# Kernel optimization log

Measured on AMD Instinct MI355X. Metric: run time of the kernel, lower is better.

## Reference

```python
import jax, jax.numpy as jnp
import numpy as np

N, T = 8192, 8192
RB, CB = 32, 32
HID = 100


def setup_inputs() -> dict:
    key = jax.random.key(0)
    ks = jax.random.split(key, 10)
    X = jax.random.normal(ks[0], (N, T), dtype=jnp.float32)
    # sorted segment ids emulate the multinomial block partition (row/col cumsum boundaries)
    row_ids = jnp.sort(jax.random.randint(ks[1], (N,), 0, RB)).astype(jnp.int32)
    col_ids = jnp.sort(jax.random.randint(ks[2], (T,), 0, CB)).astype(jnp.int32)
    d_io = RB * CB
    s1 = 1.0 / np.sqrt(d_io)
    s2 = 1.0 / np.sqrt(HID)
    W1 = jax.random.uniform(ks[3], (d_io, HID), jnp.float32, -s1, s1)
    b1 = jnp.zeros((HID,), jnp.float32)
    W2 = jax.random.uniform(ks[4], (HID, HID), jnp.float32, -s2, s2)
    b2 = jnp.zeros((HID,), jnp.float32)
    W3 = jax.random.uniform(ks[5], (HID, d_io), jnp.float32, -s2, s2)
    b3 = jnp.zeros((d_io,), jnp.float32)
    return {"X": X, "row_ids": row_ids, "col_ids": col_ids,
            "W1": W1, "b1": b1, "W2": W2, "b2": b2, "W3": W3, "b3": b3}


def _block_mean(X, row_ids, col_ids):
    # single-pass segmented reduce replacing the nested Python loop over blocks
    row_sum = jax.ops.segment_sum(X, row_ids, num_segments=RB)            # [RB, T]
    blk_sum = jax.ops.segment_sum(row_sum.T, col_ids, num_segments=CB).T  # [RB, CB]
    rcnt = jnp.bincount(row_ids, length=RB).astype(jnp.float32)
    ccnt = jnp.bincount(col_ids, length=CB).astype(jnp.float32)
    cnt = jnp.maximum(rcnt[:, None] * ccnt[None, :], 1.0)
    return blk_sum / cnt


def _mar_mlp(x_small, W1, b1, W2, b2, W3, b3):
    # 3-layer relu MLP propensity generator (MAR_missingness), sigmoid output
    h = x_small.reshape(-1)
    h = jax.nn.relu(h @ W1 + b1)
    h = jax.nn.relu(h @ W2 + b2)
    return jax.nn.sigmoid(h @ W3 + b3).reshape(RB, CB)


def reference(X, row_ids, col_ids, W1, b1, W2, b2, W3, b3):
    X_small = _block_mean(X, row_ids, col_ids)
    propensity = _mar_mlp(X_small, W1, b1, W2, b2, W3, b3)
    row_cumsum = jnp.concatenate([jnp.zeros((1,), jnp.int32),
                                  jnp.cumsum(jnp.bincount(row_ids, length=RB)).astype(jnp.int32)])
    col_cumsum = jnp.concatenate([jnp.zeros((1,), jnp.int32),
                                  jnp.cumsum(jnp.bincount(col_ids, length=CB)).astype(jnp.int32)])
    return propensity, row_cumsum, col_cumsum
```

## Files before the change

### kernel.cpp

```cpp
#include <hip/hip_runtime.h>
#include <math.h>

#define N 8192
#define T 8192
#define RB 32
#define CB 32
#define HID 100
#define DIO (RB*CB)

#define RPB 8
#define BS_BLOCKS (N / RPB)
#define K1BLOCKS 32
#define KCHUNK (DIO/K1BLOCKS)

__global__ void k_bounds(const int* __restrict__ row_ids, const int* __restrict__ col_ids,
                         int* __restrict__ rc, int* __restrict__ cc, float* __restrict__ blk) {
    int tid = blockIdx.x * blockDim.x + threadIdx.x;
    int stride = gridDim.x * blockDim.x;
    for (int i = tid; i < DIO; i += stride) blk[i] = 0.f;
    for (int i = tid; i < N; i += stride) {
        int a = row_ids[i];
        int b = (i + 1 < N) ? row_ids[i + 1] : RB;
        for (int k = a + 1; k <= b; ++k) rc[k] = i + 1;
        if (i == 0) { for (int k = 0; k <= a; ++k) rc[k] = 0; }
    }
    for (int i = tid; i < T; i += stride) {
        int a = col_ids[i];
        int b = (i + 1 < T) ? col_ids[i + 1] : CB;
        for (int k = a + 1; k <= b; ++k) cc[k] = i + 1;
        if (i == 0) { for (int k = 0; k <= a; ++k) cc[k] = 0; }
    }
}

__device__ __forceinline__ void flush_seg(float4* acc, const int4* __restrict__ col_ids4,
                                          int t, int rs, float* __restrict__ blk) {
    const int lane = t & 63;
    #pragma unroll
    for (int j = 0; j < 8; ++j) {
        int4 cs = col_ids4[t + 256 * j];
        int key = cs.x;
        float v;
        if (cs.w == key) {
            v = acc[j].x + acc[j].y + acc[j].z + acc[j].w;
        } else {
            v = acc[j].x;
            if (cs.y == key) v += acc[j].y; else atomicAdd(&blk[rs * CB + cs.y], acc[j].y);
            if (cs.z == key) v += acc[j].z; else atomicAdd(&blk[rs * CB + cs.z], acc[j].z);
            if (cs.w == key) v += acc[j].w; else atomicAdd(&blk[rs * CB + cs.w], acc[j].w);
        }
        #pragma unroll
        for (int d = 1; d < 64; d <<= 1) {
            float vv = __shfl_down(v, d, 64);
            int   kk = __shfl_down(key, d, 64);
            if (lane + d < 64 && kk == key) v += vv;
        }
        int kprev = __shfl_up(key, 1, 64);
        if (lane == 0 || kprev != key)
            atomicAdd(&blk[rs * CB + key], v);
        acc[j] = make_float4(0.f, 0.f, 0.f, 0.f);
    }
}

__global__ __launch_bounds__(256) void k_blocksum(const float* __restrict__ X,
        const int* __restrict__ row_ids, const int* __restrict__ col_ids,
        float* __restrict__ blk) {
    const int t = threadIdx.x;
    const int b = blockIdx.x;
    const int r0 = b * RPB;
    const float4* __restrict__ X4 = (const float4*)X;
    const int4*   __restrict__ C4 = (const int4*)col_ids;

    float4 acc[8];
    #pragma unroll
    for (int j = 0; j < 8; ++j) acc[j] = make_float4(0.f, 0.f, 0.f, 0.f);

    const int4* rid4 = (const int4*)(row_ids + r0);
    int4 ra = rid4[0], rb = rid4[1];

    if (ra.x == rb.w) {
        #pragma unroll
        for (int r = 0; r < RPB; ++r) {
            const float4* __restrict__ row = X4 + (size_t)(r0 + r) * (T / 4);
            #pragma unroll
            for (int j = 0; j < 8; ++j) {
                float4 x = row[t + 256 * j];
                acc[j].x += x.x; acc[j].y += x.y; acc[j].z += x.z; acc[j].w += x.w;
            }
        }
        flush_seg(acc, C4, t, ra.x, blk);
    } else {
        int rseg[RPB] = {ra.x, ra.y, ra.z, ra.w, rb.x, rb.y, rb.z, rb.w};
        int cur = rseg[0];
        for (int r = 0; r < RPB; ++r) {
            if (rseg[r] != cur) { flush_seg(acc, C4, t, cur, blk); cur = rseg[r]; }
            const float4* __restrict__ row = X4 + (size_t)(r0 + r) * (T / 4);
            #pragma unroll
            for (int j = 0; j < 8; ++j) {
                float4 x = row[t + 256 * j];
                acc[j].x += x.x; acc[j].y += x.y; acc[j].z += x.z; acc[j].w += x.w;
            }
        }
        flush_seg(acc, C4, t, cur, blk);
    }
}

__global__ __launch_bounds__(128) void k_mlp1(const float* __restrict__ blk,
        const int* __restrict__ rc, const int* __restrict__ cc,
        const float* __restrict__ W1, float* __restrict__ part1) {
    __shared__ float xs[KCHUNK];
    const int b = blockIdx.x, t = threadIdx.x;
    const int k0 = b * KCHUNK;
    if (t < KCHUNK) {
        int k = k0 + t;
        int r = k >> 5, c = k & 31;
        float cnt = fmaxf((float)(rc[r + 1] - rc[r]) * (float)(cc[c + 1] - cc[c]), 1.0f);
        xs[t] = blk[k] / cnt;
    }
    __syncthreads();
    if (t < HID) {
        float s = 0.f;
        #pragma unroll 8
        for (int kk = 0; kk < KCHUNK; ++kk)
            s += xs[kk] * W1[(size_t)(k0 + kk) * HID + t];
        part1[b * HID + t] = s;
    }
}

__global__ __launch_bounds__(128) void k_mlp2(const float* __restrict__ part1,
        const float* __restrict__ b1, const float* __restrict__ W2,
        const float* __restrict__ b2, const int* __restrict__ rc,
        const int* __restrict__ cc, float* __restrict__ h2out,
        float* __restrict__ out) {
    __shared__ float h1[HID];
    const int t = threadIdx.x;
    if (t < HID) {
        float s = b1[t];
        #pragma unroll 8
        for (int b = 0; b < K1BLOCKS; ++b) s += part1[b * HID + t];
        h1[t] = fmaxf(s, 0.f);
    }
    __syncthreads();
    if (t < HID) {
        float s = b2[t];
        #pragma unroll 4
        for (int k = 0; k < HID; ++k) s += h1[k] * W2[k * HID + t];
        h2out[t] = fmaxf(s, 0.f);
    }
    if (t < RB + 1) out[DIO + t] = (float)rc[t];
    if (t < CB + 1) out[DIO + RB + 1 + t] = (float)cc[t];
}

__global__ __launch_bounds__(128) void k_mlp3(const float* __restrict__ h2,
        const float* __restrict__ W3, const float* __restrict__ b3,
        float* __restrict__ out) {
    __shared__ float h[HID];
    const int t = threadIdx.x;
    if (t < HID) h[t] = h2[t];
    __syncthreads();
    const int o = blockIdx.x * 128 + t;
    float s = b3[o];
    #pragma unroll 4
    for (int k = 0; k < HID; ++k) s += h[k] * W3[k * DIO + o];
    out[o] = 1.f / (1.f + expf(-s));
}

extern "C" void kernel_launch(void* const* d_in, const int* in_sizes, int n_in,
                              void* d_out, int out_size, void* d_ws, size_t ws_size,
                              hipStream_t stream) {
    const float* X       = (const float*)d_in[0];
    const int*   row_ids = (const int*)  d_in[1];
    const int*   col_ids = (const int*)  d_in[2];
    const float* W1      = (const float*)d_in[3];
    const float* b1      = (const float*)d_in[4];
    const float* W2      = (const float*)d_in[5];
    const float* b2      = (const float*)d_in[6];
    const float* W3      = (const float*)d_in[7];
    const float* b3      = (const float*)d_in[8];
    float* out = (float*)d_out;

    float* blk   = (float*)d_ws;
    float* part1 = blk + DIO;
    float* h2    = part1 + K1BLOCKS * HID;
    int*   rc    = (int*)(h2 + HID);
    int*   cc    = rc + (RB + 1);

    k_bounds<<<16, 256, 0, stream>>>(row_ids, col_ids, rc, cc, blk);
    k_blocksum<<<BS_BLOCKS, 256, 0, stream>>>(X, row_ids, col_ids, blk);
    k_mlp1<<<K1BLOCKS, 128, 0, stream>>>(blk, rc, cc, W1, part1);
    k_mlp2<<<1, 128, 0, stream>>>(part1, b1, W2, b2, rc, cc, h2, out);
    k_mlp3<<<DIO / 128, 128, 0, stream>>>(h2, W3, b3, out);
}
```

Measured before the change: 425.3 us.

## Fuse MLP layers 2 and 3, replace bounds kernel with binary search and memset

Drops the separate bounds kernel. The accumulator is now cleared with hipMemsetAsync, and segment boundaries are found by binary search (lower_bound) over the sorted id arrays inside the MLP kernels. MLP layers 2 and 3 are merged into one kernel, where every block recomputes the tiny hidden layers redundantly, which saves a launch and a global round-trip. The aim is to cut launch and serialization overhead around the dominant reduction kernel, at the cost of redundant per-block work.

```diff
diff --git a/kernel.cpp b/kernel.cpp
--- a/kernel.cpp
+++ b/kernel.cpp
@@ -11,25 +11,12 @@
 #define RPB 8
 #define BS_BLOCKS (N / RPB)
 #define K1BLOCKS 32
-#define KCHUNK (DIO/K1BLOCKS)
 
-__global__ void k_bounds(const int* __restrict__ row_ids, const int* __restrict__ col_ids,
-                         int* __restrict__ rc, int* __restrict__ cc, float* __restrict__ blk) {
-    int tid = blockIdx.x * blockDim.x + threadIdx.x;
-    int stride = gridDim.x * blockDim.x;
-    for (int i = tid; i < DIO; i += stride) blk[i] = 0.f;
-    for (int i = tid; i < N; i += stride) {
-        int a = row_ids[i];
-        int b = (i + 1 < N) ? row_ids[i + 1] : RB;
-        for (int k = a + 1; k <= b; ++k) rc[k] = i + 1;
-        if (i == 0) { for (int k = 0; k <= a; ++k) rc[k] = 0; }
-    }
-    for (int i = tid; i < T; i += stride) {
-        int a = col_ids[i];
-        int b = (i + 1 < T) ? col_ids[i + 1] : CB;
-        for (int k = a + 1; k <= b; ++k) cc[k] = i + 1;
-        if (i == 0) { for (int k = 0; k <= a; ++k) cc[k] = 0; }
-    }
+__device__ __forceinline__ int lbound(const int* __restrict__ a, int n, int v) {
+    int lo = 0, hi = n;
+    #pragma unroll 1
+    while (lo < hi) { int mid = (lo + hi) >> 1; if (a[mid] < v) lo = mid + 1; else hi = mid; }
+    return lo;
 }
 
 __device__ __forceinline__ void flush_seg(float4* acc, const int4* __restrict__ col_ids4,
@@ -105,34 +92,42 @@
 }
 
 __global__ __launch_bounds__(128) void k_mlp1(const float* __restrict__ blk,
-        const int* __restrict__ rc, const int* __restrict__ cc,
+        const int* __restrict__ row_ids, const int* __restrict__ col_ids,
         const float* __restrict__ W1, float* __restrict__ part1) {
-    __shared__ float xs[KCHUNK];
+    __shared__ float xs[32];
+    __shared__ int   cb[CB + 1];
+    __shared__ int   rbnd[2];
     const int b = blockIdx.x, t = threadIdx.x;
-    const int k0 = b * KCHUNK;
-    if (t < KCHUNK) {
-        int k = k0 + t;
-        int r = k >> 5, c = k & 31;
-        float cnt = fmaxf((float)(rc[r + 1] - rc[r]) * (float)(cc[c + 1] - cc[c]), 1.0f);
-        xs[t] = blk[k] / cnt;
+
+    if (t <= CB)       cb[t]   = lbound(col_ids, T, t);
+    else if (t == 40)  rbnd[0] = lbound(row_ids, N, b);
+    else if (t == 41)  rbnd[1] = lbound(row_ids, N, b + 1);
+    __syncthreads();
+
+    if (t < 32) {
+        float cnt = fmaxf((float)(rbnd[1] - rbnd[0]) * (float)(cb[t + 1] - cb[t]), 1.0f);
+        xs[t] = blk[b * 32 + t] / cnt;
     }
     __syncthreads();
+
     if (t < HID) {
         float s = 0.f;
-        #pragma unroll 8
-        for (int kk = 0; kk < KCHUNK; ++kk)
-            s += xs[kk] * W1[(size_t)(k0 + kk) * HID + t];
+        #pragma unroll
+        for (int kk = 0; kk < 32; ++kk)
+            s += xs[kk] * W1[(size_t)(b * 32 + kk) * HID + t];
         part1[b * HID + t] = s;
     }
 }
 
-__global__ __launch_bounds__(128) void k_mlp2(const float* __restrict__ part1,
+__global__ __launch_bounds__(128) void k_mlp23(const float* __restrict__ part1,
         const float* __restrict__ b1, const float* __restrict__ W2,
-        const float* __restrict__ b2, const int* __restrict__ rc,
-        const int* __restrict__ cc, float* __restrict__ h2out,
-        float* __restrict__ out) {
+        const float* __restrict__ b2, const float* __restrict__ W3,
+        const float* __restrict__ b3, const int* __restrict__ row_ids,
+        const int* __restrict__ col_ids, float* __restrict__ out) {
     __shared__ float h1[HID];
+    __shared__ float h2[HID];
     const int t = threadIdx.x;
+
     if (t < HID) {
         float s = b1[t];
         #pragma unroll 8
@@ -140,28 +135,27 @@
         h1[t] = fmaxf(s, 0.f);
     }
     __syncthreads();
+
     if (t < HID) {
         float s = b2[t];
         #pragma unroll 4
         for (int k = 0; k < HID; ++k) s += h1[k] * W2[k * HID + t];
-        h2out[t] = fmaxf(s, 0.f);
+        h2[t] = fmaxf(s, 0.f);
     }
-    if (t < RB + 1) out[DIO + t] = (float)rc[t];
-    if (t < CB + 1) out[DIO + RB + 1 + t] = (float)cc[t];
-}
+    __syncthreads();
 
-__global__ __launch_bounds__(128) void k_mlp3(const float* __restrict__ h2,
-        const float* __restrict__ W3, const float* __restrict__ b3,
-        float* __restrict__ out) {
-    __shared__ float h[HID];
-    const int t = threadIdx.x;
-    if (t < HID) h[t] = h2[t];
-    __syncthreads();
     const int o = blockIdx.x * 128 + t;
     float s = b3[o];
     #pragma unroll 4
-    for (int k = 0; k < HID; ++k) s += h[k] * W3[k * DIO + o];
+    for (int k = 0; k < HID; ++k) s += h2[k] * W3[k * DIO + o];
     out[o] = 1.f / (1.f + expf(-s));
+
+    if (blockIdx.x == 0) {
+        if (t < RB + 1)
+            out[DIO + t] = (float)lbound(row_ids, N, t);
+        else if (t >= 64 && t < 64 + CB + 1)
+            out[DIO + RB + 1 + (t - 64)] = (float)lbound(col_ids, T, t - 64);
+    }
 }
 
 extern "C" void kernel_launch(void* const* d_in, const int* in_sizes, int n_in,
@@ -180,13 +174,10 @@
 
     float* blk   = (float*)d_ws;
     float* part1 = blk + DIO;
-    float* h2    = part1 + K1BLOCKS * HID;
-    int*   rc    = (int*)(h2 + HID);
-    int*   cc    = rc + (RB + 1);
 
-    k_bounds<<<16, 256, 0, stream>>>(row_ids, col_ids, rc, cc, blk);
+    hipMemsetAsync(blk, 0, DIO * sizeof(float), stream);
     k_blocksum<<<BS_BLOCKS, 256, 0, stream>>>(X, row_ids, col_ids, blk);
-    k_mlp1<<<K1BLOCKS, 128, 0, stream>>>(blk, rc, cc, W1, part1);
-    k_mlp2<<<1, 128, 0, stream>>>(part1, b1, W2, b2, rc, cc, h2, out);
-    k_mlp3<<<DIO / 128, 128, 0, stream>>>(h2, W3, b3, out);
+    k_mlp1<<<K1BLOCKS, 128, 0, stream>>>(blk, row_ids, col_ids, W1, part1);
+    k_mlp23<<<DIO / 128, 128, 0, stream>>>(part1, b1, W2, b2, W3, b3,
+                                           row_ids, col_ids, out);
 }
```

New measurement: 434.0 us. 2.0% more time.
